# Kernel tuning notes

Hardware: AMD Instinct MI355X
Metric: run time of the kernel (lower is better)

The kernel has to match this reference:

```python
import jax, jax.numpy as jnp
import numpy as np

DIM_M = 512
NEG_INF = -1e30


def setup_inputs() -> dict:
    key = jax.random.key(0)
    k1, k2, k3, k4, k5, k6, k7 = jax.random.split(key, 7)
    B, Lc, Lq, d = 16, 1024, 512, DIM_M
    C = jax.random.normal(k1, (B, Lc, d), dtype=jnp.float32)
    Q = jax.random.normal(k2, (B, Lq, d), dtype=jnp.float32)
    cmask = jax.random.randint(k3, (B, Lc), 0, 2).astype(jnp.float32)
    qmask = jax.random.randint(k4, (B, Lq), 0, 2).astype(jnp.float32)
    lim = np.sqrt(1.0 / d)
    w = jax.random.uniform(k5, (3 * d,), minval=-lim, maxval=lim, dtype=jnp.float32)
    # out_linear: Linear(4d -> d), torch default init
    bound = np.sqrt(1.0 / (4 * d))
    out_w = jax.random.uniform(k6, (d, 4 * d), minval=-bound, maxval=bound, dtype=jnp.float32)
    out_b = jax.random.uniform(k7, (d,), minval=-bound, maxval=bound, dtype=jnp.float32)
    return {"C": C, "Q": Q, "cmask": cmask, "qmask": qmask, "w": w, "out_w": out_w, "out_b": out_b}


def _mask_logits(t, m):
    return t * m + (1.0 - m) * NEG_INF


def reference(C, Q, cmask, qmask, w, out_w, out_b):
    d = C.shape[-1]
    w1, w2, w3 = w[:d], w[d:2 * d], w[2 * d:]
    # Decomposed trilinear similarity (same math as cat([Ct,Qt,Ct*Qt]) @ w):
    # S[b,i,j] = C[b,i]@w1 + Q[b,j]@w2 + (C[b,i]*w3) @ Q[b,j]
    S = (C @ w1)[:, :, None] + (Q @ w2)[:, None, :] \
        + jnp.einsum('bid,bjd->bij', C * w3, Q)  # [B, Lc, Lq]
    qm = qmask[:, None, :]  # [B, 1, Lq]
    cm = cmask[:, :, None]  # [B, Lc, 1]
    S1 = jax.nn.softmax(_mask_logits(S, qm), axis=2)  # over Lq
    S2 = jax.nn.softmax(_mask_logits(S, cm), axis=1)  # over Lc
    A = jnp.einsum('bij,bjd->bid', S1, Q)  # [B, Lc, d]
    # bmm(bmm(S1, S2^T), C) == S1 @ (S2^T @ C) by associativity (cheaper)
    S2TC = jnp.einsum('bij,bid->bjd', S2, C)  # [B, Lq, d]
    Bm = jnp.einsum('bij,bjd->bid', S1, S2TC)  # [B, Lc, d]
    out = jnp.concatenate([C, A, C * A, C * Bm], axis=2)  # [B, Lc, 4d]
    # dropout inactive (inference); out_linear
    return out @ out_w.T + out_b
```

## Files before the change

### kernel.cpp

```cpp
#include <hip/hip_runtime.h>
#include <hip/hip_bf16.h>


#define NB 16
#define LC 1024
#define LQ 512
#define DM 512
#define D4 2048
#define NEGINF (-1e30f)

typedef __bf16 v8bf __attribute__((ext_vector_type(8)));
typedef __bf16 v4bf __attribute__((ext_vector_type(4)));
typedef float  v4f  __attribute__((ext_vector_type(4)));

#define MFMA16 __builtin_amdgcn_mfma_f32_16x16x32_bf16

#define GLOAD16(gp, lp) __builtin_amdgcn_global_load_lds( \
    (const __attribute__((address_space(1))) void*)(gp), \
    (__attribute__((address_space(3))) void*)(lp), 16, 0, 0)

__device__ __forceinline__ void xcd_remap(int& bx, int& by, int& bz) {
  const int gx = gridDim.x, gy = gridDim.y, gz = gridDim.z;
  int flat = bx + gx * (by + gy * bz);
  int per = (gx * gy * gz) >> 3;
  int nw = (flat & 7) * per + (flat >> 3);
  bx = nw % gx;
  int r = nw / gx;
  by = r % gy;
  bz = r / gy;
}

#define P_PROLOG \
  __shared__ __bf16 Al[2][128 * 64], Bl[2][64 * 64]; \
  int bx = blockIdx.x, by = blockIdx.y, bz = blockIdx.z; \
  xcd_remap(bx, by, bz); \
  const int b = bz, i0 = by * 128, n0 = bx * 64; \
  const int t = threadIdx.x, lane = t & 63, wave = t >> 6; \
  const int wm = wave >> 1, wn = wave & 1, quad = lane >> 4, col = lane & 15; \
  const int srA = wave * 32 + (lane >> 3); \
  const int srB = wave * 16 + (lane >> 3); \
  const int swz = ((lane & 7) ^ (lane >> 3)) * 8; \
  const int q80 = ((quad ^ (col & 7)) * 8); \
  const int q81 = (((4 + quad) ^ (col & 7)) * 8); \
  v4f acc[4][2]; \
  _Pragma("unroll") for (int x = 0; x < 4; ++x) \
  _Pragma("unroll") for (int y = 0; y < 2; ++y) \
  _Pragma("unroll") for (int r = 0; r < 4; ++r) acc[x][y][r] = 0.f;

#define P_STAGE(buf, Aptr, Bptr, LDGA, LDGB, k0) \
  do { \
    _Pragma("unroll") for (int u = 0; u < 4; ++u) \
      GLOAD16((Aptr) + (size_t)(u * 8) * (LDGA) + (k0), &Al[buf][(wave * 32 + u * 8) * 64]); \
    _Pragma("unroll") for (int u = 0; u < 2; ++u) \
      GLOAD16((Bptr) + (size_t)(u * 8) * (LDGB) + (k0), &Bl[buf][(wave * 16 + u * 8) * 64]); \
  } while (0)

#define P_COMPUTE(buf) \
  do { \
    v8bf af_[4], bf_[2]; \
    _Pragma("unroll") for (int x = 0; x < 4; ++x) \
      af_[x] = *(const v8bf*)&Al[buf][(wm * 64 + x * 16 + col) * 64 + q80]; \
    _Pragma("unroll") for (int y = 0; y < 2; ++y) \
      bf_[y] = *(const v8bf*)&Bl[buf][(wn * 32 + y * 16 + col) * 64 + q80]; \
    _Pragma("unroll") for (int x = 0; x < 4; ++x) \
    _Pragma("unroll") for (int y = 0; y < 2; ++y) \
      acc[x][y] = MFMA16(af_[x], bf_[y], acc[x][y], 0, 0, 0); \
    _Pragma("unroll") for (int x = 0; x < 4; ++x) \
      af_[x] = *(const v8bf*)&Al[buf][(wm * 64 + x * 16 + col) * 64 + q81]; \
    _Pragma("unroll") for (int y = 0; y < 2; ++y) \
      bf_[y] = *(const v8bf*)&Bl[buf][(wn * 32 + y * 16 + col) * 64 + q81]; \
    _Pragma("unroll") for (int x = 0; x < 4; ++x) \
    _Pragma("unroll") for (int y = 0; y < 2; ++y) \
      acc[x][y] = MFMA16(af_[x], bf_[y], acc[x][y], 0, 0, 0); \
  } while (0)

#define P_SYNC() \
  do { asm volatile("s_waitcnt vmcnt(0)" ::: "memory"); \
       __builtin_amdgcn_s_barrier(); } while (0)

#define P_KLOOP(Arow, Brow, LDGA, LDGB, KEXT) \
  { P_STAGE(0, Arow, Brow, LDGA, LDGB, 0); \
    P_SYNC(); \
    int cur_ = 0; \
    for (int k0 = 0; k0 < (KEXT); k0 += 64) { \
      const int kn_ = k0 + 64; \
      if (kn_ < (KEXT)) P_STAGE(cur_ ^ 1, Arow, Brow, LDGA, LDGB, kn_); \
      P_COMPUTE(cur_); \
      P_SYNC(); \
      cur_ ^= 1; \
    } }

#define O_PROLOG \
  __shared__ __bf16 Al[3][128 * 32], Bl[3][128 * 32]; \
  int bx = blockIdx.x, by = blockIdx.y, bz = blockIdx.z; \
  xcd_remap(bx, by, bz); \
  const int b = bz, i0 = by * 128, n0 = bx * 128; \
  const int t = threadIdx.x, lane = t & 63, wave = t >> 6; \
  const int wm = wave >> 1, wn = wave & 1, quad = lane >> 4, col = lane & 15; \
  const int sr32 = wave * 32 + (lane >> 2); \
  const int swz = (((lane & 3) ^ ((lane >> 2) & 3) ^ ((lane >> 4) & 3)) * 8); \
  const int rdx = ((quad ^ (col & 3) ^ ((col >> 2) & 3)) * 8); \
  v4f acc[4][4]; \
  _Pragma("unroll") for (int x = 0; x < 4; ++x) \
  _Pragma("unroll") for (int y = 0; y < 4; ++y) \
  _Pragma("unroll") for (int r = 0; r < 4; ++r) acc[x][y][r] = 0.f;

#define O_STAGE(buf, Aptr, Bptr, LDGA, LDGB, k0) \
  do { \
    GLOAD16((Aptr) + (k0),                       &Al[buf][(wave * 32) * 32]); \
    GLOAD16((Aptr) + (size_t)16 * (LDGA) + (k0), &Al[buf][(wave * 32 + 16) * 32]); \
    GLOAD16((Bptr) + (k0),                       &Bl[buf][(wave * 32) * 32]); \
    GLOAD16((Bptr) + (size_t)16 * (LDGB) + (k0), &Bl[buf][(wave * 32 + 16) * 32]); \
  } while (0)

#define O_COMPUTE(buf) \
  do { \
    v8bf af_[4], bf_[4]; \
    _Pragma("unroll") for (int x = 0; x < 4; ++x) \
      af_[x] = *(const v8bf*)&Al[buf][(wm * 64 + x * 16 + col) * 32 + rdx]; \
    _Pragma("unroll") for (int y = 0; y < 4; ++y) \
      bf_[y] = *(const v8bf*)&Bl[buf][(wn * 64 + y * 16 + col) * 32 + rdx]; \
    _Pragma("unroll") for (int x = 0; x < 4; ++x) \
    _Pragma("unroll") for (int y = 0; y < 4; ++y) \
      acc[x][y] = MFMA16(af_[x], bf_[y], acc[x][y], 0, 0, 0); \
  } while (0)

#define O_SYNC4() \
  do { asm volatile("s_waitcnt vmcnt(4)" ::: "memory"); \
       __builtin_amdgcn_s_barrier(); } while (0)
#define O_SYNC0() \
  do { asm volatile("s_waitcnt vmcnt(0)" ::: "memory"); \
       __builtin_amdgcn_s_barrier(); } while (0)

#define O_ROT() do { cur_ = (cur_ == 2) ? 0 : cur_ + 1; \
                     nx2_ = (nx2_ == 2) ? 0 : nx2_ + 1; } while (0)

__global__ void k_rowdots(const float* __restrict__ C, const float* __restrict__ Q,
                          const float* __restrict__ w,
                          float* __restrict__ cw1, float* __restrict__ qw2,
                          __bf16* __restrict__ Cbf, __bf16* __restrict__ Qw3) {
  const int wid = threadIdx.x >> 6, lane = threadIdx.x & 63;
  const int row = blockIdx.x * 4 + wid;
  const bool isC = row < NB * LC;
  const int lr = isC ? row : row - NB * LC;
  const float* src = (isC ? C : Q) + (size_t)lr * DM;
  const float* wv  = isC ? w : (w + DM);
  const float* w3  = w + 2 * DM;
  __bf16* dst = (isC ? Cbf : Qw3) + (size_t)lr * DM;
  float v = 0.f;
#pragma unroll
  for (int s = 0; s < 2; ++s) {
    const int k = lane * 4 + s * 256;
    float4 f = *(const float4*)(src + k);
    float4 g = *(const float4*)(wv + k);
    v += f.x * g.x + f.y * g.y + f.z * g.z + f.w * g.w;
    v4bf h;
    if (isC) {
      h[0] = (__bf16)f.x; h[1] = (__bf16)f.y; h[2] = (__bf16)f.z; h[3] = (__bf16)f.w;
    } else {
      float4 s3 = *(const float4*)(w3 + k);
      h[0] = (__bf16)(f.x * s3.x); h[1] = (__bf16)(f.y * s3.y);
      h[2] = (__bf16)(f.z * s3.z); h[3] = (__bf16)(f.w * s3.w);
    }
    *(v4bf*)(dst + k) = h;
  }
#pragma unroll
  for (int off = 32; off; off >>= 1) v += __shfl_down(v, off, 64);
  if (lane == 0) {
    if (isC) cw1[row] = v;
    else     qw2[lr] = v;
  }
}

__device__ __forceinline__ void transpose_tile_f32(const float* __restrict__ in,
                                                   __bf16* __restrict__ outT,
                                                   int R, int Cd, int tbx, int tby, int tb) {
  __shared__ __bf16 tile[64][66];
  const int r0 = tby * 64, c0 = tbx * 64;
  const int tr = threadIdx.x >> 6, tc = threadIdx.x & 63;
  const float* inb = in + (size_t)tb * R * Cd;
  __bf16* outb = outT + (size_t)tb * Cd * R;
  for (int r = tr; r < 64; r += 4)
    tile[r][tc] = (__bf16)inb[(size_t)(r0 + r) * Cd + c0 + tc];
  __syncthreads();
  for (int c = tr; c < 64; c += 4)
    outb[(size_t)(c0 + c) * R + r0 + tc] = tile[tc][c];
}

__device__ __forceinline__ void transpose_tile_bf(const __bf16* __restrict__ in,
                                                  __bf16* __restrict__ outT,
                                                  int R, int Cd, int tbx, int tby, int tb) {
  __shared__ __bf16 tile[64][66];
  const int r0 = tby * 64, c0 = tbx * 64;
  const int tr = threadIdx.x >> 6, tc = threadIdx.x & 63;
  const __bf16* inb = in + (size_t)tb * R * Cd;
  __bf16* outb = outT + (size_t)tb * Cd * R;
  for (int r = tr; r < 64; r += 4)
    tile[r][tc] = inb[(size_t)(r0 + r) * Cd + c0 + tc];
  __syncthreads();
  for (int c = tr; c < 64; c += 4)
    outb[(size_t)(c0 + c) * R + r0 + tc] = tile[tc][c];
}

__global__ void k_prep(const float* __restrict__ C, const __bf16* __restrict__ Cbf,
                       const float* __restrict__ Q, const float* __restrict__ OW,
                       __bf16* __restrict__ CT, __bf16* __restrict__ QT,
                       __bf16* __restrict__ OWb, int use_cbf) {
  const int id = blockIdx.x;
  if (id < 2048) {
    if (use_cbf) transpose_tile_bf(Cbf, CT, LC, DM, id & 7, (id >> 3) & 15, id >> 7);
    else         transpose_tile_f32(C,  CT, LC, DM, id & 7, (id >> 3) & 15, id >> 7);
  } else if (id < 3072) {
    const int id2 = id - 2048;
    transpose_tile_f32(Q, QT, LQ, DM, id2 & 7, (id2 >> 3) & 7, id2 >> 6);
  } else {
    const size_t i = ((size_t)(id - 3072) * 256 + threadIdx.x) * 4;
    float4 f = *(const float4*)(OW + i);
    v4bf h; h[0] = (__bf16)f.x; h[1] = (__bf16)f.y; h[2] = (__bf16)f.z; h[3] = (__bf16)f.w;
    *(v4bf*)(OWb + i) = h;
  }
}

__global__ void k_cvt2b(const float* __restrict__ Cf, const float* __restrict__ OW,
                        __bf16* __restrict__ Cb3, __bf16* __restrict__ OWb) {
  const size_t NC = (size_t)NB * LC * DM;
  size_t i = ((size_t)blockIdx.x * 256 + threadIdx.x) * 4;
  if (i < NC) {
    float4 f = *(const float4*)(Cf + i);
    v4bf h; h[0] = (__bf16)f.x; h[1] = (__bf16)f.y; h[2] = (__bf16)f.z; h[3] = (__bf16)f.w;
    *(v4bf*)(Cb3 + i) = h;
  } else {
    size_t j = i - NC;
    float4 f = *(const float4*)(OW + j);
    v4bf h; h[0] = (__bf16)f.x; h[1] = (__bf16)f.y; h[2] = (__bf16)f.z; h[3] = (__bf16)f.w;
    *(v4bf*)(OWb + j) = h;
  }
}

__global__ __launch_bounds__(256) void k_mfma_S(
    const __bf16* __restrict__ Cbf, const __bf16* __restrict__ Qw3,
    const float* __restrict__ cw1, const float* __restrict__ qw2,
    float* __restrict__ S) {
  P_PROLOG
  const __bf16* Arow = Cbf + (size_t)b * LC * DM + (size_t)(i0 + srA) * DM + swz;
  const __bf16* Brow = Qw3 + (size_t)b * LQ * DM + (size_t)(n0 + srB) * DM + swz;
  P_KLOOP(Arow, Brow, DM, DM, DM)
  float* Sb = S + (size_t)b * LC * LQ;
#pragma unroll
  for (int x = 0; x < 4; ++x) {
    const int mB = i0 + wm * 64 + x * 16 + quad * 4;
    float cv[4];
#pragma unroll
    for (int r = 0; r < 4; ++r) cv[r] = cw1[b * LC + mB + r];
#pragma unroll
    for (int y = 0; y < 2; ++y) {
      const int j = n0 + wn * 32 + y * 16 + col;
      const float qv = qw2[b * LQ + j];
#pragma unroll
      for (int r = 0; r < 4; ++r)
        Sb[(size_t)(mB + r) * LQ + j] = acc[x][y][r] + cv[r] + qv;
    }
  }
}

__global__ __launch_bounds__(1024) void k_softstat(
    const float* __restrict__ S, const float* __restrict__ qmask,
    const float* __restrict__ cmask, __bf16* __restrict__ S1,
    float2* __restrict__ pstat) {
  __shared__ float2 cst[16][LQ];
  const int b = blockIdx.y, ic = blockIdx.x;
  const int tid = threadIdx.x, wv = tid >> 6, lane = tid & 63;
  const float* qm  = qmask + b * LQ;
  const float* cm  = cmask + b * LC + ic * 64;
  const float* Sb  = S  + ((size_t)b * LC + ic * 64) * LQ;
  __bf16*      S1b = S1 + ((size_t)b * LC + ic * 64) * LQ;
  float colm[8], cols[8];
#pragma unroll
  for (int tt = 0; tt < 8; ++tt) { colm[tt] = -3e38f; cols[tt] = 0.f; }
  for (int it = 0; it < 4; ++it) {
    const int r = wv * 4 + it;
    const float cmv = cm[r];
    const float* Srow = Sb + (size_t)r * LQ;
    float sv[8], l1[8];
    float m = -3e38f;
#pragma unroll
    for (int tt = 0; tt < 8; ++tt) {
      int j = lane + 64 * tt;
      sv[tt] = Srow[j];
      float qv = qm[j];
      l1[tt] = qv * sv[tt] + (1.f - qv) * NEGINF;
      m = fmaxf(m, l1[tt]);
    }
#pragma unroll
    for (int off = 32; off; off >>= 1) m = fmaxf(m, __shfl_xor(m, off, 64));
    float e[8], s = 0.f;
#pragma unroll
    for (int tt = 0; tt < 8; ++tt) { e[tt] = __expf(l1[tt] - m); s += e[tt]; }
#pragma unroll
    for (int off = 32; off; off >>= 1) s += __shfl_xor(s, off, 64);
    const float inv = 1.f / s;
#pragma unroll
    for (int tt = 0; tt < 8; ++tt)
      S1b[(size_t)r * LQ + lane + 64 * tt] = (__bf16)(e[tt] * inv);
    if (cmv != 0.f) {
#pragma unroll
      for (int tt = 0; tt < 8; ++tt) {
        float l2 = sv[tt];
        if (l2 > colm[tt]) { cols[tt] *= __expf(colm[tt] - l2); colm[tt] = l2; }
        cols[tt] += __expf(l2 - colm[tt]);
      }
    }
  }
#pragma unroll
  for (int tt = 0; tt < 8; ++tt) cst[wv][lane + 64 * tt] = make_float2(colm[tt], cols[tt]);
  __syncthreads();
  if (tid < LQ) {
    float M = -3e38f, Sd = 0.f;
#pragma unroll
    for (int k = 0; k < 16; ++k) {
      float2 p = cst[k][tid];
      float nM = fmaxf(M, p.x);
      Sd = Sd * __expf(M - nM) + p.y * __expf(p.x - nM);
      M = nM;
    }
    pstat[((size_t)(b * 16 + ic) * LQ) + tid] = make_float2(M, Sd);
  }
}

__global__ void k_colwrite(const float* __restrict__ S, const float* __restrict__ cmask,
                           const float2* __restrict__ pstat, __bf16* __restrict__ S2T) {
  __shared__ float Mf[64], If[64];
  __shared__ __bf16 tile[64][66];
  const int b = blockIdx.z, ic = blockIdx.y, j0 = blockIdx.x * 64;
  const int c = threadIdx.x & 63, ip = threadIdx.x >> 6;
  if (threadIdx.x < 64) {
    float M = -3e38f, Sd = 0.f;
#pragma unroll
    for (int k = 0; k < 16; ++k) {
      float2 p = pstat[((size_t)(b * 16 + k) * LQ) + j0 + threadIdx.x];
      float nM = fmaxf(M, p.x);
      Sd = Sd * __expf(M - nM) + p.y * __expf(p.x - nM);
      M = nM;
    }
    Mf[threadIdx.x] = M; If[threadIdx.x] = 1.f / Sd;
  }
  __syncthreads();
  const float M = Mf[c], inv = If[c];
  const float* Sb = S + ((size_t)b * LC + ic * 64) * LQ;
  const float* cm = cmask + b * LC + ic * 64;
  for (int r = ip; r < 64; r += 4) {
    if (cm[r] != 0.f)
      tile[r][c] = (__bf16)(__expf(Sb[(size_t)r * LQ + j0 + c] - M) * inv);
    else
      tile[r][c] = (__bf16)0.f;
  }
  __syncthreads();
  __bf16* S2Tb = S2T + ((size_t)b * LQ + j0) * LC + ic * 64;
  for (int jr = ip; jr < 64; jr += 4)
    S2Tb[(size_t)jr * LC + c] = tile[c][jr];
}

__global__ __launch_bounds__(256) void k_mfma_A(
    const __bf16* __restrict__ S1, const __bf16* __restrict__ QT,
    const float* __restrict__ Cf, __bf16* __restrict__ Aw, __bf16* __restrict__ CAw) {
  P_PROLOG
  const __bf16* Arow = S1 + (size_t)b * LC * LQ + (size_t)(i0 + srA) * LQ + swz;
  const __bf16* Brow = QT + (size_t)b * DM * LQ + (size_t)(n0 + srB) * LQ + swz;
  P_KLOOP(Arow, Brow, LQ, LQ, LQ)
  const float* Cb = Cf + (size_t)b * LC * DM;
  __bf16* Ab  = Aw  + (size_t)b * LC * DM;
  __bf16* CAb = CAw + (size_t)b * LC * DM;
#pragma unroll
  for (int x = 0; x < 4; ++x) {
    const int mB = i0 + wm * 64 + x * 16 + quad * 4;
#pragma unroll
    for (int y = 0; y < 2; ++y) {
      const int n = n0 + wn * 32 + y * 16 + col;
#pragma unroll
      for (int r = 0; r < 4; ++r) {
        const float av = acc[x][y][r];
        const float cv = Cb[(size_t)(mB + r) * DM + n];
        Ab[(size_t)(mB + r) * DM + n]  = (__bf16)av;
        CAb[(size_t)(mB + r) * DM + n] = (__bf16)(av * cv);
      }
    }
  }
}

__global__ __launch_bounds__(256) void k_mfma_T(
    const __bf16* __restrict__ S2T, const __bf16* __restrict__ CT, __bf16* __restrict__ S2TCT) {
  P_PROLOG
  const int j0 = i0;
  const __bf16* Arow = S2T + (size_t)b * LQ * LC + (size_t)(j0 + srA) * LC + swz;
  const __bf16* Brow = CT  + (size_t)b * DM * LC + (size_t)(n0 + srB) * LC + swz;
  P_KLOOP(Arow, Brow, LC, LC, LC)
#pragma unroll
  for (int x = 0; x < 4; ++x) {
    const int jB = j0 + wm * 64 + x * 16 + quad * 4;
#pragma unroll
    for (int y = 0; y < 2; ++y) {
      const int n = n0 + wn * 32 + y * 16 + col;
      v4bf h;
#pragma unroll
      for (int r = 0; r < 4; ++r) h[r] = (__bf16)acc[x][y][r];
      *(v4bf*)&S2TCT[((size_t)b * DM + n) * LQ + jB] = h;
    }
  }
}

__global__ __launch_bounds__(256) void k_mfma_Bm(
    const __bf16* __restrict__ S1, const __bf16* __restrict__ S2TCT,
    const float* __restrict__ Cf, __bf16* __restrict__ CBw) {
  P_PROLOG
  const __bf16* Arow = S1    + (size_t)b * LC * LQ + (size_t)(i0 + srA) * LQ + swz;
  const __bf16* Brow = S2TCT + (size_t)b * DM * LQ + (size_t)(n0 + srB) * LQ + swz;
  P_KLOOP(Arow, Brow, LQ, LQ, LQ)
  const float* Cb = Cf + (size_t)b * LC * DM;
  __bf16* CBb = CBw + (size_t)b * LC * DM;
#pragma unroll
  for (int x = 0; x < 4; ++x) {
    const int mB = i0 + wm * 64 + x * 16 + quad * 4;
#pragma unroll
    for (int y = 0; y < 2; ++y) {
      const int n = n0 + wn * 32 + y * 16 + col;
#pragma unroll
      for (int r = 0; r < 4; ++r) {
        const float cv = Cb[(size_t)(mB + r) * DM + n];
        CBb[(size_t)(mB + r) * DM + n] = (__bf16)(acc[x][y][r] * cv);
      }
    }
  }
}

__global__ __launch_bounds__(256) void k_mfma_out(
    const __bf16* __restrict__ Cb3, const __bf16* __restrict__ Aw,
    const __bf16* __restrict__ CAw, const __bf16* __restrict__ CBw,
    const __bf16* __restrict__ OWb, const float* __restrict__ ob,
    float* __restrict__ out) {
  O_PROLOG
  const size_t rowoff = (size_t)b * LC * DM + (size_t)(i0 + sr32) * DM + swz;
  const __bf16* Aseg[4] = {Cb3 + rowoff, Aw + rowoff, CAw + rowoff, CBw + rowoff};
  const __bf16* Brow0 = OWb + (size_t)(n0 + sr32) * D4 + swz;
  O_STAGE(0, Aseg[0], Brow0, DM, D4, 0);
  O_STAGE(1, Aseg[0], Brow0, DM, D4, 32);
  O_SYNC4();
  int cur_ = 0, nx2_ = 2;
#pragma unroll
  for (int seg = 0; seg < 4; ++seg) {
    const __bf16* Ac = Aseg[seg];
    const __bf16* An = Aseg[seg < 3 ? seg + 1 : 3];
    const __bf16* Bc = Brow0 + seg * DM;
    const __bf16* Bn = Brow0 + (seg < 3 ? seg + 1 : 3) * DM;
    for (int j = 0; j < 14; ++j) {
      O_STAGE(nx2_, Ac, Bc, DM, D4, (j + 2) * 32);
      O_COMPUTE(cur_);
      O_SYNC4();
      O_ROT();
    }
    if (seg < 3) {
      O_STAGE(nx2_, An, Bn, DM, D4, 0);
      O_COMPUTE(cur_);
      O_SYNC4();
      O_ROT();
      O_STAGE(nx2_, An, Bn, DM, D4, 32);
      O_COMPUTE(cur_);
      O_SYNC4();
      O_ROT();
    } else {
      O_COMPUTE(cur_);
      O_SYNC0();
      O_ROT();
      O_COMPUTE(cur_);
    }
  }
  float* outb = out + (size_t)b * LC * DM;
#pragma unroll
  for (int x = 0; x < 4; ++x) {
    const int mB = i0 + wm * 64 + x * 16 + quad * 4;
#pragma unroll
    for (int y = 0; y < 4; ++y) {
      const int n = n0 + wn * 64 + y * 16 + col;
      const float bv = ob[n];
#pragma unroll
      for (int r = 0; r < 4; ++r)
        outb[(size_t)(mB + r) * DM + n] = acc[x][y][r] + bv;
    }
  }
}

extern "C" void kernel_launch(void* const* d_in, const int* in_sizes, int n_in,
                              void* d_out, int out_size, void* d_ws, size_t ws_size,
                              hipStream_t stream) {
  const float* C     = (const float*)d_in[0];
  const float* Q     = (const float*)d_in[1];
  const float* cmask = (const float*)d_in[2];
  const float* qmask = (const float*)d_in[3];
  const float* w     = (const float*)d_in[4];
  const float* out_w = (const float*)d_in[5];
  const float* out_b = (const float*)d_in[6];
  float* out = (float*)d_out;

  char* base = (char*)d_ws;
  float*  cw1   = (float*)base;
  float*  qw2   = (float*)(base + 65536);
  char*   R     = base + 131072;
  float*  S     = (float*)R;
  __bf16* CT    = (__bf16*)R;
  __bf16* Aw    = (__bf16*)R;
  __bf16* QT    = (__bf16*)(R + (16u << 20));
  __bf16* CBw   = (__bf16*)(R + (16u << 20));
  __bf16* S1    = (__bf16*)(R + (32u << 20));
  __bf16* Qw3   = (__bf16*)(R + (48u << 20));
  __bf16* S2T   = (__bf16*)(R + (48u << 20));
  __bf16* CAw   = (__bf16*)(R + (48u << 20));
  float2* pstat = (float2*)(R + (64u << 20));
  __bf16* S2TCT = (__bf16*)(R + (64u << 20));
  (void)in_sizes; (void)n_in; (void)out_size;

  const size_t need_big = 131072 + (90ull << 20);
  const bool bigws = ws_size >= need_big;

  __bf16 *Cbf, *Cbf3, *OWbf;
  if (bigws) {
    Cbf  = (__bf16*)(R + (72u << 20));
    Cbf3 = Cbf;
    OWbf = (__bf16*)(R + (88u << 20));
  } else {
    Cbf  = (__bf16*)(R + (32u << 20));
    Cbf3 = (__bf16*)(R + (32u << 20));
    OWbf = (__bf16*)(R + (64u << 20));
  }

  k_rowdots<<<(NB * LC + NB * LQ) / 4, 256, 0, stream>>>(C, Q, w, cw1, qw2, Cbf, Qw3);
  k_mfma_S<<<dim3(LQ / 64, LC / 128, NB), 256, 0, stream>>>(Cbf, Qw3, cw1, qw2, S);
  k_softstat<<<dim3(LC / 64, NB), 1024, 0, stream>>>(S, qmask, cmask, S1, pstat);
  k_colwrite<<<dim3(LQ / 64, LC / 64, NB), 256, 0, stream>>>(S, cmask, pstat, S2T);
  k_prep<<<bigws ? 4096 : 3072, 256, 0, stream>>>(C, Cbf, Q, out_w, CT, QT, OWbf,
                                                  bigws ? 1 : 0);
  k_mfma_T<<<dim3(DM / 64, LQ / 128, NB), 256, 0, stream>>>(S2T, CT, S2TCT);
  k_mfma_A<<<dim3(DM / 64, LC / 128, NB), 256, 0, stream>>>(S1, QT, C, Aw, CAw);
  k_mfma_Bm<<<dim3(DM / 64, LC / 128, NB), 256, 0, stream>>>(S1, S2TCT, C, CBw);
  if (!bigws)
    k_cvt2b<<<(NB * LC * DM + DM * D4) / 1024, 256, 0, stream>>>(C, out_w, Cbf3, OWbf);
  k_mfma_out<<<dim3(DM / 128, LC / 128, NB), 256, 0, stream>>>(Cbf3, Aw, CAw, CBw, OWbf, out_b, out);
}
```

Measured before the change: 273.8 us.

## Switch P-kernel K loop to three-stage pipeline with 32-wide K tiles

The P-type GEMM tiles shrink from 64-wide to 32-wide K slices and move from double to triple buffering in LDS. Loads run two stages ahead, and the wait uses vmcnt(3) so the next stage's loads can stay in flight across the barrier. LDS addressing and the swizzle are rewritten to match the O-kernel's 32-wide layout. The aim is to hide global-to-LDS latency better, at the cost of twice as many barriers and fewer MFMAs per sync.

```diff
diff --git a/kernel.cpp b/kernel.cpp
--- a/kernel.cpp
+++ b/kernel.cpp
@@ -31,17 +31,16 @@
 }
 
 #define P_PROLOG \
-  __shared__ __bf16 Al[2][128 * 64], Bl[2][64 * 64]; \
+  __shared__ __bf16 Al[3][128 * 32], Bl[3][64 * 32]; \
   int bx = blockIdx.x, by = blockIdx.y, bz = blockIdx.z; \
   xcd_remap(bx, by, bz); \
   const int b = bz, i0 = by * 128, n0 = bx * 64; \
   const int t = threadIdx.x, lane = t & 63, wave = t >> 6; \
   const int wm = wave >> 1, wn = wave & 1, quad = lane >> 4, col = lane & 15; \
-  const int srA = wave * 32 + (lane >> 3); \
-  const int srB = wave * 16 + (lane >> 3); \
-  const int swz = ((lane & 7) ^ (lane >> 3)) * 8; \
-  const int q80 = ((quad ^ (col & 7)) * 8); \
-  const int q81 = (((4 + quad) ^ (col & 7)) * 8); \
+  const int srA = wave * 32 + (lane >> 2); \
+  const int srB = wave * 16 + (lane >> 2); \
+  const int swz = (((lane & 3) ^ ((lane >> 2) & 3) ^ ((lane >> 4) & 3)) * 8); \
+  const int rdx = ((quad ^ (col & 3) ^ ((col >> 2) & 3)) * 8); \
   v4f acc[4][2]; \
   _Pragma("unroll") for (int x = 0; x < 4; ++x) \
   _Pragma("unroll") for (int y = 0; y < 2; ++y) \
@@ -49,45 +48,51 @@
 
 #define P_STAGE(buf, Aptr, Bptr, LDGA, LDGB, k0) \
   do { \
-    _Pragma("unroll") for (int u = 0; u < 4; ++u) \
-      GLOAD16((Aptr) + (size_t)(u * 8) * (LDGA) + (k0), &Al[buf][(wave * 32 + u * 8) * 64]); \
-    _Pragma("unroll") for (int u = 0; u < 2; ++u) \
-      GLOAD16((Bptr) + (size_t)(u * 8) * (LDGB) + (k0), &Bl[buf][(wave * 16 + u * 8) * 64]); \
+    GLOAD16((Aptr) + (k0),                       &Al[buf][(wave * 32) * 32]); \
+    GLOAD16((Aptr) + (size_t)16 * (LDGA) + (k0), &Al[buf][(wave * 32 + 16) * 32]); \
+    GLOAD16((Bptr) + (k0),                       &Bl[buf][(wave * 16) * 32]); \
   } while (0)
 
 #define P_COMPUTE(buf) \
   do { \
     v8bf af_[4], bf_[2]; \
     _Pragma("unroll") for (int x = 0; x < 4; ++x) \
-      af_[x] = *(const v8bf*)&Al[buf][(wm * 64 + x * 16 + col) * 64 + q80]; \
+      af_[x] = *(const v8bf*)&Al[buf][(wm * 64 + x * 16 + col) * 32 + rdx]; \
     _Pragma("unroll") for (int y = 0; y < 2; ++y) \
-      bf_[y] = *(const v8bf*)&Bl[buf][(wn * 32 + y * 16 + col) * 64 + q80]; \
-    _Pragma("unroll") for (int x = 0; x < 4; ++x) \
-    _Pragma("unroll") for (int y = 0; y < 2; ++y) \
-      acc[x][y] = MFMA16(af_[x], bf_[y], acc[x][y], 0, 0, 0); \
-    _Pragma("unroll") for (int x = 0; x < 4; ++x) \
-      af_[x] = *(const v8bf*)&Al[buf][(wm * 64 + x * 16 + col) * 64 + q81]; \
-    _Pragma("unroll") for (int y = 0; y < 2; ++y) \
-      bf_[y] = *(const v8bf*)&Bl[buf][(wn * 32 + y * 16 + col) * 64 + q81]; \
+      bf_[y] = *(const v8bf*)&Bl[buf][(wn * 32 + y * 16 + col) * 32 + rdx]; \
     _Pragma("unroll") for (int x = 0; x < 4; ++x) \
     _Pragma("unroll") for (int y = 0; y < 2; ++y) \
       acc[x][y] = MFMA16(af_[x], bf_[y], acc[x][y], 0, 0, 0); \
   } while (0)
 
-#define P_SYNC() \
+#define P_SYNC3() \
+  do { asm volatile("s_waitcnt vmcnt(3)" ::: "memory"); \
+       __builtin_amdgcn_s_barrier(); } while (0)
+#define P_SYNC0() \
   do { asm volatile("s_waitcnt vmcnt(0)" ::: "memory"); \
        __builtin_amdgcn_s_barrier(); } while (0)
 
+#define P_ROT() do { cur_ = (cur_ == 2) ? 0 : cur_ + 1; \
+                     nx2_ = (nx2_ == 2) ? 0 : nx2_ + 1; } while (0)
+
 #define P_KLOOP(Arow, Brow, LDGA, LDGB, KEXT) \
   { P_STAGE(0, Arow, Brow, LDGA, LDGB, 0); \
-    P_SYNC(); \
-    int cur_ = 0; \
-    for (int k0 = 0; k0 < (KEXT); k0 += 64) { \
+    P_STAGE(1, Arow, Brow, LDGA, LDGB, 32); \
+    P_SYNC3(); \
+    int cur_ = 0, nx2_ = 2; \
+    for (int k0 = 0; k0 < (KEXT); k0 += 32) { \
       const int kn_ = k0 + 64; \
-      if (kn_ < (KEXT)) P_STAGE(cur_ ^ 1, Arow, Brow, LDGA, LDGB, kn_); \
-      P_COMPUTE(cur_); \
-      P_SYNC(); \
-      cur_ ^= 1; \
+      if (kn_ < (KEXT)) { \
+        P_STAGE(nx2_, Arow, Brow, LDGA, LDGB, kn_); \
+        P_COMPUTE(cur_); \
+        P_SYNC3(); \
+      } else if (k0 + 32 < (KEXT)) { \
+        P_COMPUTE(cur_); \
+        P_SYNC0(); \
+      } else { \
+        P_COMPUTE(cur_); \
+      } \
+      P_ROT(); \
     } }
 
 #define O_PROLOG \
```

Result: no change. 269.4 us, median of 2 (-1.6%).
